# Performance work log

Hardware: AMD Instinct MI355X
Metric: run time of the kernel (lower is better)

Reference implementation:

```python
import jax, jax.numpy as jnp
import numpy as np


def setup_inputs() -> dict:
    key = jax.random.key(0)
    ks = jax.random.split(key, 12)
    B, S, D, Q = 16, 2048, 1024, 64
    std = 1.0 / np.sqrt(D)
    return {
        "raw": jax.random.normal(ks[0], (B, S, D), jnp.float32),
        "post_dec": jax.random.normal(ks[1], (B, S, D), jnp.float32),
        "mask": jnp.ones((B, S), dtype=bool),
        "questions": jax.random.uniform(ks[2], (Q, D), jnp.float32),
        "Wk": jax.random.normal(ks[3], (D, D), jnp.float32) * std,
        "bk": jnp.zeros((D,), jnp.float32),
        "Wi": jax.random.normal(ks[4], (1, D), jnp.float32) * std,
        "bi": jnp.zeros((1,), jnp.float32),
        "Wo": jax.random.normal(ks[5], (D, D), jnp.float32) * std,
        "bo": jnp.zeros((D,), jnp.float32),
        "Wu1": jax.random.normal(ks[6], (1, D), jnp.float32) * std,
        "bu1": jnp.zeros((1,), jnp.float32),
        "Wu2": jax.random.normal(ks[7], (1, D), jnp.float32) * std,
        "bu2": jnp.zeros((1,), jnp.float32),
        "b1": jax.random.uniform(ks[8], (1,), jnp.float32),
    }


def reference(raw, post_dec, mask, questions, Wk, bk, Wi, bi, Wo, bo, Wu1, bu1, Wu2, bu2, b1):
    D = raw.shape[-1]
    Q = questions.shape[0]
    inv_sqrt_d = jnp.float32(1.0 / np.sqrt(D))
    inv_sqrt_q = jnp.float32(1.0 / np.sqrt(Q))

    # ---- create_A_matrix: write external memory A [Q, D] ----
    k = raw @ Wk.T + bk                                   # [B,S,D]
    v = raw * jax.nn.sigmoid(raw @ Wi.T + bi)             # ignore gate, [B,S,D]
    scores = jnp.einsum('qd,bsd->bqs', questions, k) * inv_sqrt_d  # [B,Q,S]
    scores = jnp.where(mask[:, None, :], scores, jnp.float32(-1e9))
    attn = jax.nn.softmax(scores, axis=-1)
    A = jnp.einsum('bqs,bsd->qd', attn, v) / jnp.float32(raw.shape[0])  # mean over batch

    # ---- get_data_from_A_matrix: read memory ----
    ko = post_dec @ Wo.T + bo                              # [B,S,D]
    s2 = jnp.einsum('bsd,qd->bsq', ko, questions) * inv_sqrt_q  # [B,S,Q]
    A2 = jax.nn.softmax(s2, axis=-1) @ A                   # [B,S,D]
    gate = jax.nn.sigmoid((post_dec @ Wu1.T + bu1) + (A2 @ Wu2.T + bu2) + b1)  # [B,S,1]
    return post_dec + A2 * gate
```

## Files before the change

kernel.cpp:

```cpp
#include <hip/hip_runtime.h>
#include <math.h>

#define NBATCH 16
#define SEQ    2048
#define BS     32768
#define DIM    1024
#define NQ     64
#define CKS    68
#define INV_SQRT_D 0.03125f
#define INV_SQRT_Q 0.125f

#define OFF_QT   0
#define OFF_CKT  65536
#define OFF_COT  135168
#define OFF_S1   204800
#define OFF_G2   2334720
#define OFF_A    2367488
#define OFF_BO   2433024
#define OFF_AW   2433088
#define OFF_CKP  2433152
#define OFF_COP  2474112
#define OFF_W2B  2515072
#define OFF_AMT  3563648

typedef short bf16x8 __attribute__((ext_vector_type(8)));
typedef float f32x4 __attribute__((ext_vector_type(4)));

union V8 { uint4 u4; bf16x8 s8; uint32_t u[4]; };

__device__ __forceinline__ f32x4 mfma16(bf16x8 a, bf16x8 b, f32x4 c) {
  return __builtin_amdgcn_mfma_f32_16x16x32_bf16(a, b, c, 0, 0, 0);
}
__device__ __forceinline__ uint32_t f2b(float f) { return __float_as_uint(f); }
__device__ __forceinline__ uint32_t packtr(float lo, float hi) {
  return __builtin_amdgcn_perm(f2b(hi), f2b(lo), 0x07060302u);
}
__device__ __forceinline__ uint32_t rne1(float f) {
  uint32_t u = f2b(f);
  return (u + 0x7FFFu + ((u >> 16) & 1u)) >> 16;
}
__device__ __forceinline__ uint32_t packrne(float lo, float hi) {
  return rne1(lo) | (rne1(hi) << 16);
}
__device__ __forceinline__ bf16x8 ldg8(const unsigned short* p) {
  V8 v; v.u4 = *(const uint4*)p; return v.s8;
}
__device__ __forceinline__ bf16x8 pack8(const float* p) {
  float4 a = *(const float4*)p;
  float4 b = *(const float4*)(p + 4);
  V8 v;
  v.u[0] = packtr(a.x, a.y);
  v.u[1] = packtr(a.z, a.w);
  v.u[2] = packtr(b.x, b.y);
  v.u[3] = packtr(b.z, b.w);
  return v.s8;
}

__global__ __launch_bounds__(256) void kpre(const float* __restrict__ questions,
                                            const float* __restrict__ bo,
                                            const float* __restrict__ Wi,
                                            const float* __restrict__ Wu1,
                                            float* __restrict__ ws) {
  __shared__ float red[4];
  float* qT    = ws + OFF_QT;
  float* CKT   = ws + OFF_CKT;
  float* COT   = ws + OFF_COT;
  float* biasO = ws + OFF_BO;
  int bid = blockIdx.x, tid = threadIdx.x;
  if (bid < 64) {
    int q = bid;
    float acc = 0.f;
    for (int e = tid; e < DIM; e += 256) {
      float v = questions[q*DIM + e];
      qT[e*NQ + q] = v;
      acc += v * bo[e];
    }
    for (int off = 32; off > 0; off >>= 1) acc += __shfl_xor(acc, off, 64);
    if ((tid & 63) == 0) red[tid >> 6] = acc;
    __syncthreads();
    if (tid == 0) biasO[q] = red[0] + red[1] + red[2] + red[3];
  } else {
    int r = bid - 64;
    int h = r & 1;
    const float* src = (r < 2) ? Wi : Wu1;
    float* dst = (r < 2) ? CKT : COT;
    int d = h*512 + tid;
    dst[d*CKS + 64] = src[d];
    d += 256;
    dst[d*CKS + 64] = src[d];
  }
}

__global__ __launch_bounds__(256) void k0_proj(const float* __restrict__ Wk,
                                               const float* __restrict__ Wo,
                                               float* __restrict__ ws) {
  const float* qT = ws + OFF_QT;
  int bid = blockIdx.x;
  int mat = bid & 1;
  int kc  = (bid >> 1) & 3;
  int dt  = bid >> 3;
  const float* W = mat ? Wo : Wk;
  float* dest = ws + (mat ? OFF_COT : OFF_CKT);
  int d0 = dt * 64, e0 = kc * 256;
  __shared__ __align__(16) float aL[32*CKS];
  __shared__ __align__(16) float bL[32*CKS];
  int tid = threadIdx.x;
  int tx = tid & 15, ty = tid >> 4;
  float acc[4][4] = {};
  for (int ek = e0; ek < e0 + 256; ek += 32) {
    for (int idx = tid; idx < 32*64; idx += 256) {
      int kk = idx >> 6, j = idx & 63;
      aL[kk*CKS + j] = qT[(ek + kk)*NQ + j];
      bL[kk*CKS + j] = W[(size_t)(ek + kk)*DIM + d0 + j];
    }
    __syncthreads();
#pragma unroll
    for (int kk = 0; kk < 32; kk++) {
      float4 av = *(const float4*)&aL[kk*CKS + ty*4];
      float4 bv = *(const float4*)&bL[kk*CKS + tx*4];
      float a[4] = {av.x, av.y, av.z, av.w};
      float b[4] = {bv.x, bv.y, bv.z, bv.w};
#pragma unroll
      for (int r = 0; r < 4; ++r)
#pragma unroll
        for (int c = 0; c < 4; ++c)
          acc[r][c] += a[r] * b[c];
    }
    __syncthreads();
  }
#pragma unroll
  for (int r = 0; r < 4; ++r)
#pragma unroll
    for (int c = 0; c < 4; ++c)
      atomicAdd(&dest[(d0 + tx*4 + c)*CKS + ty*4 + r], acc[r][c]);
}

__global__ __launch_bounds__(256) void kpack(float* __restrict__ ws) {
  int bid = blockIdx.x;
  int row = bid % 80;
  int mat = bid / 80;
  const float* src = ws + (mat ? OFF_COT : OFF_CKT);
  unsigned short* dst = (unsigned short*)(ws + (mat ? OFF_COP : OFF_CKP));
  int d = threadIdx.x * 4;
  float v[4];
#pragma unroll
  for (int i = 0; i < 4; ++i)
    v[i] = (row <= 64) ? src[(d + i)*CKS + row] : 0.f;
  uint2 o;
  o.x = packrne(v[0], v[1]);
  o.y = packrne(v[2], v[3]);
  *(uint2*)(dst + (size_t)row*DIM + d) = o;
}

__global__ __launch_bounds__(256) void k1_scores(const float* __restrict__ raw,
                                                 float* __restrict__ ws) {
  const unsigned short* CKp = (const unsigned short*)(ws + OFF_CKP);
  float* S1 = ws + OFF_S1;
  int tid = threadIdx.x;
  int wave = tid >> 6, lane = tid & 63, lm = lane & 15, quad = lane >> 4;
  int bid = blockIdx.x;
  int kh = bid & 1;
  int tb = (bid >> 1) * 64 + wave * 16;
  f32x4 acc[5] = {};
  int k0beg = kh * 512;
  for (int k0 = k0beg; k0 < k0beg + 512; k0 += 32) {
    bf16x8 bfr = pack8(raw + (size_t)(tb + lm)*DIM + k0 + quad*8);
#pragma unroll
    for (int mt = 0; mt < 5; ++mt) {
      bf16x8 af = ldg8(CKp + (size_t)(mt*16 + lm)*DIM + k0 + quad*8);
      acc[mt] = mfma16(af, bfr, acc[mt]);
    }
  }
#pragma unroll
  for (int mt = 0; mt < 4; ++mt)
#pragma unroll
    for (int reg = 0; reg < 4; ++reg)
      atomicAdd(&S1[(size_t)(mt*16 + quad*4 + reg)*BS + tb + lm], acc[mt][reg]);
  if (quad == 0)
    atomicAdd(&S1[(size_t)64*BS + tb + lm], acc[4][0]);
}

__global__ __launch_bounds__(256) void k2g(const float* __restrict__ biP,
                                           float* __restrict__ ws) {
  const float* S1 = ws + OFF_S1;
  float* g2 = ws + OFF_G2;
  int t = blockIdx.x*256 + threadIdx.x;
  float v = S1[(size_t)64*BS + t] + biP[0];
  g2[t] = (1.f / (1.f + __expf(-v))) * (1.f / (float)NBATCH);
}

__global__ __launch_bounds__(256) void k2_softmax(float* __restrict__ ws) {
  const float* S1 = ws + OFF_S1;
  const float* g2 = ws + OFF_G2;
  uint32_t* w2u = (uint32_t*)(ws + OFF_W2B);
  __shared__ float redA[4];
  __shared__ float redB[4];
  int bid = blockIdx.x;
  int q = bid & 63, b = bid >> 6;
  int tid = threadIdx.x, wave = tid >> 6, lane = tid & 63;
  const float* row = S1 + (size_t)q*BS + b*SEQ + tid*8;
  float4 xa = *(const float4*)row;
  float4 xb = *(const float4*)(row + 4);
  float x[8] = {xa.x, xa.y, xa.z, xa.w, xb.x, xb.y, xb.z, xb.w};
#pragma unroll
  for (int i = 0; i < 8; ++i) x[i] *= INV_SQRT_D;
  float m = -1e30f;
#pragma unroll
  for (int i = 0; i < 8; ++i) m = fmaxf(m, x[i]);
  for (int off = 32; off > 0; off >>= 1) m = fmaxf(m, __shfl_xor(m, off, 64));
  if (lane == 0) redA[wave] = m;
  __syncthreads();
  m = fmaxf(fmaxf(redA[0], redA[1]), fmaxf(redA[2], redA[3]));
  float e[8];
  float s = 0.f;
#pragma unroll
  for (int i = 0; i < 8; ++i) { e[i] = __expf(x[i] - m); s += e[i]; }
  for (int off = 32; off > 0; off >>= 1) s += __shfl_xor(s, off, 64);
  if (lane == 0) redB[wave] = s;
  __syncthreads();
  s = redB[0] + redB[1] + redB[2] + redB[3];
  float inv = 1.f / s;
  const float* g2b = g2 + b*SEQ + tid*8;
  float4 ga = *(const float4*)g2b;
  float4 gb = *(const float4*)(g2b + 4);
  float g[8] = {ga.x, ga.y, ga.z, ga.w, gb.x, gb.y, gb.z, gb.w};
  float w[8];
#pragma unroll
  for (int i = 0; i < 8; ++i) w[i] = e[i] * inv * g[i];
  uint4 o;
  o.x = packtr(w[0], w[1]);
  o.y = packtr(w[2], w[3]);
  o.z = packtr(w[4], w[5]);
  o.w = packtr(w[6], w[7]);
  *(uint4*)&w2u[((size_t)q*BS + b*SEQ + tid*8) >> 1] = o;
}

#define K3STR 36
__global__ __launch_bounds__(256) void k3_accA(const float* __restrict__ raw,
                                               float* __restrict__ ws) {
  const unsigned short* w2b = (const unsigned short*)(ws + OFF_W2B);
  float* A = ws + OFF_A;
  int bid = blockIdx.x;
  int dt = bid & 7, tc = bid >> 3;
  int d0 = dt*128;
  int tid = threadIdx.x;
  int wave = tid >> 6, lane = tid & 63, lm = lane & 15, quad = lane >> 4;
  int pq = tid & 7;
  int dr = tid >> 3;
  __shared__ __align__(16) uint32_t ldsB[128*K3STR];
  f32x4 acc[4][2] = {};
  for (int tk = tc*512; tk < tc*512 + 512; tk += 64) {
    float4 rv[8];
#pragma unroll
    for (int r = 0; r < 8; ++r)
      rv[r] = *(const float4*)&raw[(size_t)(tk + pq*8 + r)*DIM + d0 + dr*4];
    __syncthreads();
    int pc = ((pq ^ (dr & 7)) << 2);
#pragma unroll
    for (int j = 0; j < 4; ++j) {
      const float* f0 = (const float*)&rv[0];
      uint4 wv;
      wv.x = packtr(((const float*)&rv[0])[j], ((const float*)&rv[1])[j]);
      wv.y = packtr(((const float*)&rv[2])[j], ((const float*)&rv[3])[j]);
      wv.z = packtr(((const float*)&rv[4])[j], ((const float*)&rv[5])[j]);
      wv.w = packtr(((const float*)&rv[6])[j], ((const float*)&rv[7])[j]);
      (void)f0;
      *(uint4*)&ldsB[(dr*4 + j)*K3STR + pc] = wv;
    }
    __syncthreads();
#pragma unroll
    for (int ks = 0; ks < 2; ++ks) {
      bf16x8 af[4];
#pragma unroll
      for (int mt = 0; mt < 4; ++mt)
        af[mt] = ldg8(w2b + (size_t)(mt*16 + lm)*BS + tk + ks*32 + quad*8);
      bf16x8 bfr[2];
#pragma unroll
      for (int nt = 0; nt < 2; ++nt) {
        int rowd = wave*32 + nt*16 + lm;
        int pcr = (((ks*4 + quad) ^ ((rowd >> 2) & 7)) << 2);
        V8 v; v.u4 = *(const uint4*)&ldsB[rowd*K3STR + pcr];
        bfr[nt] = v.s8;
      }
#pragma unroll
      for (int mt = 0; mt < 4; ++mt)
#pragma unroll
        for (int nt = 0; nt < 2; ++nt)
          acc[mt][nt] = mfma16(af[mt], bfr[nt], acc[mt][nt]);
    }
  }
#pragma unroll
  for (int mt = 0; mt < 4; ++mt)
#pragma unroll
    for (int nt = 0; nt < 2; ++nt)
#pragma unroll
      for (int reg = 0; reg < 4; ++reg)
        atomicAdd(&A[(mt*16 + quad*4 + reg)*DIM + d0 + wave*32 + nt*16 + lm],
                  acc[mt][nt][reg]);
}

__global__ __launch_bounds__(256) void k3b_aw(const float* __restrict__ Wu2,
                                              float* __restrict__ ws) {
  const float* A = ws + OFF_A;
  float* aw = ws + OFF_AW;
  unsigned short* at = (unsigned short*)(ws + OFF_AMT);
  __shared__ float red[4];
  int q = blockIdx.x, tid = threadIdx.x;
  float acc = 0.f;
  for (int d = tid; d < DIM; d += 256) {
    float v = A[q*DIM + d];
    acc += v * Wu2[d];
    at[(size_t)d*NQ + q] = (unsigned short)rne1(v);
  }
  for (int off = 32; off > 0; off >>= 1) acc += __shfl_xor(acc, off, 64);
  if ((tid & 63) == 0) red[tid >> 6] = acc;
  __syncthreads();
  if (tid == 0) aw[q] = red[0] + red[1] + red[2] + red[3];
}

#define T4STR 85
#define WSTR  72
#define BM4   32
__global__ __launch_bounds__(256) void k4_phase2(const float* __restrict__ post_dec,
                                                 const float* __restrict__ bu1p,
                                                 const float* __restrict__ bu2p,
                                                 const float* __restrict__ b1p,
                                                 float* __restrict__ out,
                                                 float* __restrict__ ws) {
  const unsigned short* COp = (const unsigned short*)(ws + OFF_COP);
  const unsigned short* AmT = (const unsigned short*)(ws + OFF_AMT);
  const float* biasO = ws + OFF_BO;
  const float* aw    = ws + OFF_AW;
  __shared__ __align__(16) float T[2][BM4][T4STR];
  __shared__ __align__(16) unsigned short wL[BM4*WSTR];
  __shared__ float gateL[BM4], bOL[64], awL[64];
  int t0 = blockIdx.x * BM4;
  int tid = threadIdx.x;
  int wave = tid >> 6, lane = tid & 63, lm = lane & 15, quad = lane >> 4;
  if (tid < 64) { bOL[tid] = biasO[tid]; awL[tid] = aw[tid]; }

  int mh = wave & 1;
  int kh = wave >> 1;
  f32x4 acc[5] = {};
  for (int k0 = kh*512; k0 < kh*512 + 512; k0 += 32) {
    bf16x8 af = pack8(post_dec + (size_t)(t0 + mh*16 + lm)*DIM + k0 + quad*8);
#pragma unroll
    for (int nt = 0; nt < 5; ++nt) {
      bf16x8 b = ldg8(COp + (size_t)(nt*16 + lm)*DIM + k0 + quad*8);
      acc[nt] = mfma16(af, b, acc[nt]);
    }
  }
#pragma unroll
  for (int nt = 0; nt < 5; ++nt)
#pragma unroll
    for (int reg = 0; reg < 4; ++reg)
      T[kh][mh*16 + quad*4 + reg][nt*16 + lm] = acc[nt][reg];
  __syncthreads();

  {
    int row = tid >> 3, sub = tid & 7;
    const float* T0 = T[0][row];
    const float* T1 = T[1][row];
    float x[8];
#pragma unroll
    for (int i = 0; i < 8; ++i) {
      int j = sub*8 + i;
      x[i] = (T0[j] + T1[j] + bOL[j]) * INV_SQRT_Q;
    }
    float m = x[0];
#pragma unroll
    for (int i = 1; i < 8; ++i) m = fmaxf(m, x[i]);
    for (int off = 1; off < 8; off <<= 1) m = fmaxf(m, __shfl_xor(m, off, 64));
    float e[8], s = 0.f, sa = 0.f;
#pragma unroll
    for (int i = 0; i < 8; ++i) {
      e[i] = __expf(x[i] - m);
      s += e[i];
      sa += e[i] * awL[sub*8 + i];
    }
    for (int off = 1; off < 8; off <<= 1) {
      s  += __shfl_xor(s, off, 64);
      sa += __shfl_xor(sa, off, 64);
    }
    float inv = 1.f / s;
    uint32_t* wr = (uint32_t*)(wL + row*WSTR);
#pragma unroll
    for (int i2 = 0; i2 < 4; ++i2)
      wr[sub*4 + i2] = packtr(e[2*i2]*inv, e[2*i2+1]*inv);
    if (sub == 0) {
      float u1 = T0[64] + T1[64];
      float u2 = sa * inv;
      float garg = u1 + bu1p[0] + u2 + bu2p[0] + b1p[0];
      gateL[row] = 1.f / (1.f + __expf(-garg));
    }
  }
  __syncthreads();

  float gv[2][4];
#pragma unroll
  for (int mt = 0; mt < 2; ++mt)
#pragma unroll
    for (int reg = 0; reg < 4; ++reg)
      gv[mt][reg] = gateL[mt*16 + quad*4 + reg];
  for (int d0 = 0; d0 < DIM; d0 += 256) {
    f32x4 acc2[2][4] = {};
#pragma unroll
    for (int ks = 0; ks < 2; ++ks) {
      bf16x8 am[2];
#pragma unroll
      for (int mt = 0; mt < 2; ++mt) {
        V8 v; v.u4 = *(const uint4*)&wL[(mt*16 + lm)*WSTR + ks*32 + quad*8];
        am[mt] = v.s8;
      }
      bf16x8 bn[4];
#pragma unroll
      for (int nt = 0; nt < 4; ++nt)
        bn[nt] = ldg8(AmT + (size_t)(d0 + wave*64 + nt*16 + lm)*NQ + ks*32 + quad*8);
#pragma unroll
      for (int mt = 0; mt < 2; ++mt)
#pragma unroll
        for (int nt = 0; nt < 4; ++nt)
          acc2[mt][nt] = mfma16(am[mt], bn[nt], acc2[mt][nt]);
    }
#pragma unroll
    for (int mt = 0; mt < 2; ++mt)
#pragma unroll
      for (int nt = 0; nt < 4; ++nt)
#pragma unroll
        for (int reg = 0; reg < 4; ++reg) {
          int t = t0 + mt*16 + quad*4 + reg;
          int d = d0 + wave*64 + nt*16 + lm;
          out[(size_t)t*DIM + d] = post_dec[(size_t)t*DIM + d]
                                 + acc2[mt][nt][reg] * gv[mt][reg];
        }
  }
}

extern "C" void kernel_launch(void* const* d_in, const int* in_sizes, int n_in,
                              void* d_out, int out_size, void* d_ws, size_t ws_size,
                              hipStream_t stream) {
  const float* raw       = (const float*)d_in[0];
  const float* post_dec  = (const float*)d_in[1];
  const float* questions = (const float*)d_in[3];
  const float* Wk        = (const float*)d_in[4];
  const float* Wi        = (const float*)d_in[6];
  const float* bi        = (const float*)d_in[7];
  const float* Wo        = (const float*)d_in[8];
  const float* bo        = (const float*)d_in[9];
  const float* Wu1       = (const float*)d_in[10];
  const float* bu1       = (const float*)d_in[11];
  const float* Wu2       = (const float*)d_in[12];
  const float* bu2       = (const float*)d_in[13];
  const float* b1        = (const float*)d_in[14];
  float* out = (float*)d_out;
  float* ws  = (float*)d_ws;

  hipMemsetAsync(ws + OFF_CKT, 0, (size_t)2*DIM*CKS*sizeof(float), stream);
  hipMemsetAsync(ws + OFF_S1,  0, (size_t)65*BS*sizeof(float), stream);
  hipMemsetAsync(ws + OFF_A,   0, (size_t)NQ*DIM*sizeof(float), stream);

  kpre<<<68, 256, 0, stream>>>(questions, bo, Wi, Wu1, ws);
  k0_proj<<<128, 256, 0, stream>>>(Wk, Wo, ws);
  kpack<<<160, 256, 0, stream>>>(ws);
  k1_scores<<<1024, 256, 0, stream>>>(raw, ws);
  k2g<<<128, 256, 0, stream>>>(bi, ws);
  k2_softmax<<<1024, 256, 0, stream>>>(ws);
  k3_accA<<<512, 256, 0, stream>>>(raw, ws);
  k3b_aw<<<64, 256, 0, stream>>>(Wu2, ws);
  k4_phase2<<<1024, 256, 0, stream>>>(post_dec, bu1, bu2, b1, out, ws);
}
```

Measured before the change: 597.8 us.

## Drop split-K in score kernels, remove atomics and S1 memset, make k4 per-wave

k1_scores now has each block cover the full K dimension for 64 tokens, so it writes S1 with plain stores. That removes the atomicAdd and the large S1 memset. k3_accA doubles the token chunk per block and halves the grid. k4_phase2 is restructured so each wave owns 16 tokens end to end: full-K projection, softmax in per-wave LDS, then the A2 GEMM over all D, with no block-wide barriers. Grids halve, which may lower occupancy and parallelism, while avoiding atomics, memset traffic and synchronisation.

Result: faster. 554.9 us (-7.2%).

```diff
diff --git a/kernel.cpp b/kernel.cpp
--- a/kernel.cpp
+++ b/kernel.cpp
@@ -158,12 +158,9 @@
   float* S1 = ws + OFF_S1;
   int tid = threadIdx.x;
   int wave = tid >> 6, lane = tid & 63, lm = lane & 15, quad = lane >> 4;
-  int bid = blockIdx.x;
-  int kh = bid & 1;
-  int tb = (bid >> 1) * 64 + wave * 16;
+  int tb = blockIdx.x*64 + wave*16;
   f32x4 acc[5] = {};
-  int k0beg = kh * 512;
-  for (int k0 = k0beg; k0 < k0beg + 512; k0 += 32) {
+  for (int k0 = 0; k0 < DIM; k0 += 32) {
     bf16x8 bfr = pack8(raw + (size_t)(tb + lm)*DIM + k0 + quad*8);
 #pragma unroll
     for (int mt = 0; mt < 5; ++mt) {
@@ -175,9 +172,9 @@
   for (int mt = 0; mt < 4; ++mt)
 #pragma unroll
     for (int reg = 0; reg < 4; ++reg)
-      atomicAdd(&S1[(size_t)(mt*16 + quad*4 + reg)*BS + tb + lm], acc[mt][reg]);
+      S1[(size_t)(mt*16 + quad*4 + reg)*BS + tb + lm] = acc[mt][reg];
   if (quad == 0)
-    atomicAdd(&S1[(size_t)64*BS + tb + lm], acc[4][0]);
+    S1[(size_t)64*BS + tb + lm] = acc[4][0];
 }
 
 __global__ __launch_bounds__(256) void k2g(const float* __restrict__ biP,
@@ -249,7 +246,7 @@
   int dr = tid >> 3;
   __shared__ __align__(16) uint32_t ldsB[128*K3STR];
   f32x4 acc[4][2] = {};
-  for (int tk = tc*512; tk < tc*512 + 512; tk += 64) {
+  for (int tk = tc*1024; tk < tc*1024 + 1024; tk += 64) {
     float4 rv[8];
 #pragma unroll
     for (int r = 0; r < 8; ++r)
@@ -318,9 +315,8 @@
   if (tid == 0) aw[q] = red[0] + red[1] + red[2] + red[3];
 }
 
-#define T4STR 85
-#define WSTR  72
-#define BM4   32
+#define T4S  67
+#define W4SU 36
 __global__ __launch_bounds__(256) void k4_phase2(const float* __restrict__ post_dec,
                                                  const float* __restrict__ bu1p,
                                                  const float* __restrict__ bu2p,
@@ -331,108 +327,90 @@
   const unsigned short* AmT = (const unsigned short*)(ws + OFF_AMT);
   const float* biasO = ws + OFF_BO;
   const float* aw    = ws + OFF_AW;
-  __shared__ __align__(16) float T[2][BM4][T4STR];
-  __shared__ __align__(16) unsigned short wL[BM4*WSTR];
-  __shared__ float gateL[BM4], bOL[64], awL[64];
-  int t0 = blockIdx.x * BM4;
+  __shared__ __align__(16) float    Tall[4][16*T4S];
+  __shared__ __align__(16) uint32_t wAll[4][16*W4SU];
+  __shared__ float gAll[4][16];
   int tid = threadIdx.x;
   int wave = tid >> 6, lane = tid & 63, lm = lane & 15, quad = lane >> 4;
-  if (tid < 64) { bOL[tid] = biasO[tid]; awL[tid] = aw[tid]; }
-
-  int mh = wave & 1;
-  int kh = wave >> 1;
+  int t0 = blockIdx.x*64 + wave*16;
+
   f32x4 acc[5] = {};
-  for (int k0 = kh*512; k0 < kh*512 + 512; k0 += 32) {
-    bf16x8 af = pack8(post_dec + (size_t)(t0 + mh*16 + lm)*DIM + k0 + quad*8);
-#pragma unroll
-    for (int nt = 0; nt < 5; ++nt) {
-      bf16x8 b = ldg8(COp + (size_t)(nt*16 + lm)*DIM + k0 + quad*8);
-      acc[nt] = mfma16(af, b, acc[nt]);
-    }
-  }
-#pragma unroll
-  for (int nt = 0; nt < 5; ++nt)
+  for (int k0 = 0; k0 < DIM; k0 += 32) {
+    bf16x8 b = pack8(post_dec + (size_t)(t0 + lm)*DIM + k0 + quad*8);
+#pragma unroll
+    for (int mt = 0; mt < 5; ++mt) {
+      bf16x8 a = ldg8(COp + (size_t)(mt*16 + lm)*DIM + k0 + quad*8);
+      acc[mt] = mfma16(a, b, acc[mt]);
+    }
+  }
+  float* Tw = Tall[wave];
+#pragma unroll
+  for (int mt = 0; mt < 4; ++mt)
 #pragma unroll
     for (int reg = 0; reg < 4; ++reg)
-      T[kh][mh*16 + quad*4 + reg][nt*16 + lm] = acc[nt][reg];
-  __syncthreads();
+      Tw[lm*T4S + mt*16 + quad*4 + reg] = acc[mt][reg];
+  if (quad == 0) Tw[lm*T4S + 64] = acc[4][0];
 
   {
-    int row = tid >> 3, sub = tid & 7;
-    const float* T0 = T[0][row];
-    const float* T1 = T[1][row];
-    float x[8];
-#pragma unroll
-    for (int i = 0; i < 8; ++i) {
-      int j = sub*8 + i;
-      x[i] = (T0[j] + T1[j] + bOL[j]) * INV_SQRT_Q;
-    }
+    int r = lane >> 2, h = lane & 3;
+    float x[16];
+#pragma unroll
+    for (int i = 0; i < 16; ++i)
+      x[i] = (Tw[r*T4S + h*16 + i] + biasO[h*16 + i]) * INV_SQRT_Q;
     float m = x[0];
 #pragma unroll
-    for (int i = 1; i < 8; ++i) m = fmaxf(m, x[i]);
-    for (int off = 1; off < 8; off <<= 1) m = fmaxf(m, __shfl_xor(m, off, 64));
-    float e[8], s = 0.f, sa = 0.f;
-#pragma unroll
-    for (int i = 0; i < 8; ++i) {
+    for (int i = 1; i < 16; ++i) m = fmaxf(m, x[i]);
+    m = fmaxf(m, __shfl_xor(m, 1, 64));
+    m = fmaxf(m, __shfl_xor(m, 2, 64));
+    float e[16], s = 0.f, sa = 0.f;
+#pragma unroll
+    for (int i = 0; i < 16; ++i) {
       e[i] = __expf(x[i] - m);
       s += e[i];
-      sa += e[i] * awL[sub*8 + i];
-    }
-    for (int off = 1; off < 8; off <<= 1) {
-      s  += __shfl_xor(s, off, 64);
-      sa += __shfl_xor(sa, off, 64);
-    }
+      sa += e[i] * aw[h*16 + i];
+    }
+    s  += __shfl_xor(s, 1, 64);  s  += __shfl_xor(s, 2, 64);
+    sa += __shfl_xor(sa, 1, 64); sa += __shfl_xor(sa, 2, 64);
     float inv = 1.f / s;
-    uint32_t* wr = (uint32_t*)(wL + row*WSTR);
-#pragma unroll
-    for (int i2 = 0; i2 < 4; ++i2)
-      wr[sub*4 + i2] = packtr(e[2*i2]*inv, e[2*i2+1]*inv);
-    if (sub == 0) {
-      float u1 = T0[64] + T1[64];
-      float u2 = sa * inv;
-      float garg = u1 + bu1p[0] + u2 + bu2p[0] + b1p[0];
-      gateL[row] = 1.f / (1.f + __expf(-garg));
-    }
-  }
-  __syncthreads();
-
-  float gv[2][4];
-#pragma unroll
-  for (int mt = 0; mt < 2; ++mt)
-#pragma unroll
-    for (int reg = 0; reg < 4; ++reg)
-      gv[mt][reg] = gateL[mt*16 + quad*4 + reg];
-  for (int d0 = 0; d0 < DIM; d0 += 256) {
-    f32x4 acc2[2][4] = {};
+    uint32_t* wr = wAll[wave] + r*W4SU + h*8;
+#pragma unroll
+    for (int i2 = 0; i2 < 8; ++i2)
+      wr[i2] = packtr(e[2*i2]*inv, e[2*i2+1]*inv);
+    if (h == 0) {
+      float garg = Tw[r*T4S + 64] + bu1p[0] + sa*inv + bu2p[0] + b1p[0];
+      gAll[wave][r] = 1.f / (1.f + __expf(-garg));
+    }
+  }
+
+  const unsigned short* wS = (const unsigned short*)wAll[wave];
+  bf16x8 am[2];
+#pragma unroll
+  for (int ks = 0; ks < 2; ++ks) {
+    V8 v; v.u4 = *(const uint4*)&wS[lm*(W4SU*2) + ks*32 + quad*8];
+    am[ks] = v.s8;
+  }
+  float gv[4];
+#pragma unroll
+  for (int reg = 0; reg < 4; ++reg) gv[reg] = gAll[wave][quad*4 + reg];
+  for (int d0 = 0; d0 < DIM; d0 += 64) {
+    f32x4 acc2[4] = {};
 #pragma unroll
     for (int ks = 0; ks < 2; ++ks) {
-      bf16x8 am[2];
-#pragma unroll
-      for (int mt = 0; mt < 2; ++mt) {
-        V8 v; v.u4 = *(const uint4*)&wL[(mt*16 + lm)*WSTR + ks*32 + quad*8];
-        am[mt] = v.s8;
+#pragma unroll
+      for (int nt = 0; nt < 4; ++nt) {
+        bf16x8 bn = ldg8(AmT + (size_t)(d0 + nt*16 + lm)*NQ + ks*32 + quad*8);
+        acc2[nt] = mfma16(am[ks], bn, acc2[nt]);
       }
-      bf16x8 bn[4];
-#pragma unroll
-      for (int nt = 0; nt < 4; ++nt)
-        bn[nt] = ldg8(AmT + (size_t)(d0 + wave*64 + nt*16 + lm)*NQ + ks*32 + quad*8);
-#pragma unroll
-      for (int mt = 0; mt < 2; ++mt)
-#pragma unroll
-        for (int nt = 0; nt < 4; ++nt)
-          acc2[mt][nt] = mfma16(am[mt], bn[nt], acc2[mt][nt]);
-    }
-#pragma unroll
-    for (int mt = 0; mt < 2; ++mt)
-#pragma unroll
-      for (int nt = 0; nt < 4; ++nt)
-#pragma unroll
-        for (int reg = 0; reg < 4; ++reg) {
-          int t = t0 + mt*16 + quad*4 + reg;
-          int d = d0 + wave*64 + nt*16 + lm;
-          out[(size_t)t*DIM + d] = post_dec[(size_t)t*DIM + d]
-                                 + acc2[mt][nt][reg] * gv[mt][reg];
-        }
+    }
+#pragma unroll
+    for (int nt = 0; nt < 4; ++nt)
+#pragma unroll
+      for (int reg = 0; reg < 4; ++reg) {
+        int t = t0 + quad*4 + reg;
+        int d = d0 + nt*16 + lm;
+        out[(size_t)t*DIM + d] = post_dec[(size_t)t*DIM + d]
+                               + acc2[nt][reg] * gv[reg];
+      }
   }
 }
 
@@ -456,16 +434,15 @@
   float* ws  = (float*)d_ws;
 
   hipMemsetAsync(ws + OFF_CKT, 0, (size_t)2*DIM*CKS*sizeof(float), stream);
-  hipMemsetAsync(ws + OFF_S1,  0, (size_t)65*BS*sizeof(float), stream);
   hipMemsetAsync(ws + OFF_A,   0, (size_t)NQ*DIM*sizeof(float), stream);
 
   kpre<<<68, 256, 0, stream>>>(questions, bo, Wi, Wu1, ws);
   k0_proj<<<128, 256, 0, stream>>>(Wk, Wo, ws);
   kpack<<<160, 256, 0, stream>>>(ws);
-  k1_scores<<<1024, 256, 0, stream>>>(raw, ws);
+  k1_scores<<<512, 256, 0, stream>>>(raw, ws);
   k2g<<<128, 256, 0, stream>>>(bi, ws);
   k2_softmax<<<1024, 256, 0, stream>>>(ws);
-  k3_accA<<<512, 256, 0, stream>>>(raw, ws);
+  k3_accA<<<256, 256, 0, stream>>>(raw, ws);
   k3b_aw<<<64, 256, 0, stream>>>(Wu2, ws);
-  k4_phase2<<<1024, 256, 0, stream>>>(post_dec, bu1, bu2, b1, out, ws);
-}
+  k4_phase2<<<512, 256, 0, stream>>>(post_dec, bu1, bu2, b1, out, ws);
+}
```
